# Optimization experiments

Measured on AMD Instinct MI355X. Metric: run time of the kernel, lower is better.

Reference implementation:

```python
import jax, jax.numpy as jnp
import numpy as np

B, T, D = 32, 4096, 512


def setup_inputs() -> dict:
    key = jax.random.key(0)
    k1, k2, k3 = jax.random.split(key, 3)
    inp = jax.random.normal(k1, (B, T, D), dtype=jnp.float32)
    # lengths in [1, T] so every row has at least one valid position
    lens = jax.random.randint(k2, (B,), 1, T + 1, dtype=jnp.int32)
    # matches nn.init.uniform_(slot_embedding, -1/d_hid, 1/d_hid)
    slot_embedding = jax.random.uniform(k3, (D,), dtype=jnp.float32,
                                        minval=-1.0 / D, maxval=1.0 / D)
    return {"inp": inp, "lens": lens, "slot_embedding": slot_embedding}


def reference(inp, lens, slot_embedding):
    # dropout p=0.0 -> identity (eval semantics)
    # scores[b, t] = <inp[b, t, :], slot_embedding>  -> [B, T]
    scores = jnp.einsum("btd,d->bt", inp, slot_embedding)
    # mask padded positions (t >= lens[b]) with -inf, as the per-sample loop does
    valid = jnp.arange(inp.shape[1], dtype=lens.dtype)[None, :] < lens[:, None]  # [B, T]
    scores = jnp.where(valid, scores, -jnp.inf)
    weights = jax.nn.softmax(scores, axis=1)  # [B, T]
    # context[b, d] = sum_t weights[b, t] * inp[b, t, d]
    context = jnp.einsum("bt,btd->bd", weights, inp)
    return context
```

## Files before the change

kernel.cpp:

```cpp
#include <hip/hip_runtime.h>
#include <math.h>


#define BB 32
#define TT 4096
#define DD 512

__global__ __launch_bounds__(256) void
slot_partial_kernel(const float* __restrict__ inp,
                    const int* __restrict__ lens,
                    const float* __restrict__ slot,
                    float* __restrict__ m_arr,
                    float* __restrict__ l_arr,
                    float* __restrict__ c_arr,
                    int CH, int R) {
    const int chunk = blockIdx.x;
    const int b     = blockIdx.y;
    const int tid   = threadIdx.x;
    const int wave  = tid >> 6;
    const int lane  = tid & 63;
    const int p     = b * CH + chunk;

    const int len = lens[b];
    const int cs  = chunk * R;
    const int ce  = min(cs + R, len);

    const float4 s0 = *reinterpret_cast<const float4*>(slot + lane * 4);
    const float4 s1 = *reinterpret_cast<const float4*>(slot + 256 + lane * 4);

    float  m = -INFINITY;
    float  l = 0.0f;
    float4 c0 = make_float4(0.f, 0.f, 0.f, 0.f);
    float4 c1 = make_float4(0.f, 0.f, 0.f, 0.f);

    const size_t baseB = (size_t)b * TT * DD;

    int t = cs + wave;
    if (t < ce) {
        const float* rp = inp + baseB + (size_t)t * DD;
        float4 a0 = *reinterpret_cast<const float4*>(rp + lane * 4);
        float4 a1 = *reinterpret_cast<const float4*>(rp + 256 + lane * 4);
        while (t < ce) {
            const int tn = t + 4;
            float4 n0, n1;
            if (tn < ce) {
                const float* rn = inp + baseB + (size_t)tn * DD;
                n0 = *reinterpret_cast<const float4*>(rn + lane * 4);
                n1 = *reinterpret_cast<const float4*>(rn + 256 + lane * 4);
            }
            float part = a0.x * s0.x + a0.y * s0.y + a0.z * s0.z + a0.w * s0.w
                       + a1.x * s1.x + a1.y * s1.y + a1.z * s1.z + a1.w * s1.w;
            #pragma unroll
            for (int off = 32; off >= 1; off >>= 1)
                part += __shfl_xor(part, off, 64);
            const float s = part;

            if (s > m) {
                const float alpha = __expf(m - s);
                l *= alpha;
                c0.x *= alpha; c0.y *= alpha; c0.z *= alpha; c0.w *= alpha;
                c1.x *= alpha; c1.y *= alpha; c1.z *= alpha; c1.w *= alpha;
                m = s;
            }
            const float w = __expf(s - m);
            l += w;
            c0.x += w * a0.x; c0.y += w * a0.y; c0.z += w * a0.z; c0.w += w * a0.w;
            c1.x += w * a1.x; c1.y += w * a1.y; c1.z += w * a1.z; c1.w += w * a1.w;

            a0 = n0; a1 = n1;
            t = tn;
        }
    }

    __shared__ float sm[4];
    __shared__ float sl[4];
    __shared__ float sc[4][DD];

    if (lane == 0) { sm[wave] = m; sl[wave] = l; }
    *reinterpret_cast<float4*>(&sc[wave][lane * 4])       = c0;
    *reinterpret_cast<float4*>(&sc[wave][256 + lane * 4]) = c1;
    __syncthreads();

    const float M = fmaxf(fmaxf(sm[0], sm[1]), fmaxf(sm[2], sm[3]));
    float aw[4];
    float L = 0.0f;
    #pragma unroll
    for (int w = 0; w < 4; ++w) {
        aw[w] = (sm[w] == -INFINITY) ? 0.0f : __expf(sm[w] - M);
        L += sl[w] * aw[w];
    }

    for (int d = tid; d < DD; d += 256) {
        const float acc = sc[0][d] * aw[0] + sc[1][d] * aw[1]
                        + sc[2][d] * aw[2] + sc[3][d] * aw[3];
        c_arr[(size_t)p * DD + d] = acc;
    }
    if (tid == 0) { m_arr[p] = M; l_arr[p] = L; }
}

__global__ __launch_bounds__(256) void
slot_combine_kernel(const float* __restrict__ m_arr,
                    const float* __restrict__ l_arr,
                    const float* __restrict__ c_arr,
                    float* __restrict__ out,
                    int CH) {
    const int b   = blockIdx.x;
    const int tid = threadIdx.x;

    __shared__ float sAlpha[64];

    float M = -INFINITY;
    for (int j = 0; j < CH; ++j) M = fmaxf(M, m_arr[b * CH + j]);

    if (tid < CH) {
        const float mj = m_arr[b * CH + tid];
        sAlpha[tid] = (mj == -INFINITY) ? 0.0f : __expf(mj - M);
    }
    __syncthreads();

    float L = 0.0f;
    for (int j = 0; j < CH; ++j) L += l_arr[b * CH + j] * sAlpha[j];
    const float invL = 1.0f / L;

    for (int d = tid; d < DD; d += 256) {
        float acc = 0.0f;
        for (int j = 0; j < CH; ++j)
            acc += c_arr[((size_t)b * CH + j) * DD + d] * sAlpha[j];
        out[b * DD + d] = acc * invL;
    }
}

extern "C" void kernel_launch(void* const* d_in, const int* in_sizes, int n_in,
                              void* d_out, int out_size, void* d_ws, size_t ws_size,
                              hipStream_t stream) {
    const float* inp  = (const float*)d_in[0];
    const int*   lens = (const int*)d_in[1];
    const float* slot = (const float*)d_in[2];
    float* out = (float*)d_out;

    int CH = 32;
    while (CH > 1 && (size_t)BB * CH * (2 + DD) * sizeof(float) > ws_size)
        CH >>= 1;
    const int R = TT / CH;
    const int P = BB * CH;

    float* m_arr = (float*)d_ws;
    float* l_arr = m_arr + P;
    float* c_arr = l_arr + P;

    dim3 grid1(CH, BB, 1);
    slot_partial_kernel<<<grid1, 256, 0, stream>>>(inp, lens, slot,
                                                   m_arr, l_arr, c_arr, CH, R);
    slot_combine_kernel<<<BB, 256, 0, stream>>>(m_arr, l_arr, c_arr, out, CH);
}
```

Before: 335.4 us.

## Give each wave a contiguous row range and process four rows per iteration

Each wave now takes a contiguous sub-range of the chunk instead of interleaved rows. It loads four rows at a time with a one-group-ahead prefetch and batches their four shuffle reductions together, applying the online-softmax rescale once per group. The chunk count rises to 64 to give more blocks, and the combine kernel switches to float2 loads. The goal is more memory-level parallelism and fewer serial shuffle and exp dependency chains, at the cost of higher register pressure. Combine work also grows with the larger chunk count.

Measured after the change: 334.7 us. No clear change (-0.2%).

```diff
diff --git a/kernel.cpp b/kernel.cpp
--- a/kernel.cpp
+++ b/kernel.cpp
@@ -13,7 +13,7 @@
                     float* __restrict__ m_arr,
                     float* __restrict__ l_arr,
                     float* __restrict__ c_arr,
-                    int CH, int R) {
+                    int CH, int R, int RW) {
     const int chunk = blockIdx.x;
     const int b     = blockIdx.y;
     const int tid   = threadIdx.x;
@@ -23,7 +23,8 @@
 
     const int len = lens[b];
     const int cs  = chunk * R;
-    const int ce  = min(cs + R, len);
+    const int ws_start = cs + wave * RW;
+    const int ws_end   = min(ws_start + RW, len);
 
     const float4 s0 = *reinterpret_cast<const float4*>(slot + lane * 4);
     const float4 s1 = *reinterpret_cast<const float4*>(slot + 256 + lane * 4);
@@ -33,42 +34,66 @@
     float4 c0 = make_float4(0.f, 0.f, 0.f, 0.f);
     float4 c1 = make_float4(0.f, 0.f, 0.f, 0.f);
 
-    const size_t baseB = (size_t)b * TT * DD;
+    const float* bp = inp + (size_t)b * TT * DD;
 
-    int t = cs + wave;
-    if (t < ce) {
-        const float* rp = inp + baseB + (size_t)t * DD;
-        float4 a0 = *reinterpret_cast<const float4*>(rp + lane * 4);
-        float4 a1 = *reinterpret_cast<const float4*>(rp + 256 + lane * 4);
-        while (t < ce) {
-            const int tn = t + 4;
-            float4 n0, n1;
-            if (tn < ce) {
-                const float* rn = inp + baseB + (size_t)tn * DD;
-                n0 = *reinterpret_cast<const float4*>(rn + lane * 4);
-                n1 = *reinterpret_cast<const float4*>(rn + 256 + lane * 4);
+    if (ws_start < ws_end) {
+        float4 a[4][2];
+        #pragma unroll
+        for (int r = 0; r < 4; ++r) {
+            const int t = min(ws_start + r, ws_end - 1);
+            const float* rp = bp + (size_t)t * DD + lane * 4;
+            a[r][0] = *reinterpret_cast<const float4*>(rp);
+            a[r][1] = *reinterpret_cast<const float4*>(rp + 256);
+        }
+        for (int g = ws_start; g < ws_end; g += 4) {
+            const int gn = g + 4;
+            float4 n[4][2];
+            if (gn < ws_end) {
+                #pragma unroll
+                for (int r = 0; r < 4; ++r) {
+                    const int t = min(gn + r, ws_end - 1);
+                    const float* rp = bp + (size_t)t * DD + lane * 4;
+                    n[r][0] = *reinterpret_cast<const float4*>(rp);
+                    n[r][1] = *reinterpret_cast<const float4*>(rp + 256);
+                }
             }
-            float part = a0.x * s0.x + a0.y * s0.y + a0.z * s0.z + a0.w * s0.w
-                       + a1.x * s1.x + a1.y * s1.y + a1.z * s1.z + a1.w * s1.w;
+            float sd[4];
             #pragma unroll
-            for (int off = 32; off >= 1; off >>= 1)
-                part += __shfl_xor(part, off, 64);
-            const float s = part;
+            for (int r = 0; r < 4; ++r) {
+                sd[r] = a[r][0].x * s0.x + a[r][0].y * s0.y
+                      + a[r][0].z * s0.z + a[r][0].w * s0.w
+                      + a[r][1].x * s1.x + a[r][1].y * s1.y
+                      + a[r][1].z * s1.z + a[r][1].w * s1.w;
+            }
+            #pragma unroll
+            for (int off = 32; off >= 1; off >>= 1) {
+                #pragma unroll
+                for (int r = 0; r < 4; ++r)
+                    sd[r] += __shfl_xor(sd[r], off, 64);
+            }
+            #pragma unroll
+            for (int r = 0; r < 4; ++r)
+                if (g + r >= ws_end) sd[r] = -INFINITY;
 
-            if (s > m) {
-                const float alpha = __expf(m - s);
+            const float gmax = fmaxf(fmaxf(sd[0], sd[1]), fmaxf(sd[2], sd[3]));
+            if (gmax > m) {
+                const float alpha = __expf(m - gmax);
                 l *= alpha;
                 c0.x *= alpha; c0.y *= alpha; c0.z *= alpha; c0.w *= alpha;
                 c1.x *= alpha; c1.y *= alpha; c1.z *= alpha; c1.w *= alpha;
-                m = s;
+                m = gmax;
             }
-            const float w = __expf(s - m);
-            l += w;
-            c0.x += w * a0.x; c0.y += w * a0.y; c0.z += w * a0.z; c0.w += w * a0.w;
-            c1.x += w * a1.x; c1.y += w * a1.y; c1.z += w * a1.z; c1.w += w * a1.w;
-
-            a0 = n0; a1 = n1;
-            t = tn;
+            #pragma unroll
+            for (int r = 0; r < 4; ++r) {
+                const float w = __expf(sd[r] - m);
+                l += w;
+                c0.x += w * a[r][0].x; c0.y += w * a[r][0].y;
+                c0.z += w * a[r][0].z; c0.w += w * a[r][0].w;
+                c1.x += w * a[r][1].x; c1.y += w * a[r][1].y;
+                c1.z += w * a[r][1].z; c1.w += w * a[r][1].w;
+            }
+            #pragma unroll
+            for (int r = 0; r < 4; ++r) { a[r][0] = n[r][0]; a[r][1] = n[r][1]; }
         }
     }
 
@@ -107,7 +132,7 @@
     const int b   = blockIdx.x;
     const int tid = threadIdx.x;
 
-    __shared__ float sAlpha[64];
+    __shared__ float sAlpha[256];
 
     float M = -INFINITY;
     for (int j = 0; j < CH; ++j) M = fmaxf(M, m_arr[b * CH + j]);
@@ -122,12 +147,16 @@
     for (int j = 0; j < CH; ++j) L += l_arr[b * CH + j] * sAlpha[j];
     const float invL = 1.0f / L;
 
-    for (int d = tid; d < DD; d += 256) {
-        float acc = 0.0f;
-        for (int j = 0; j < CH; ++j)
-            acc += c_arr[((size_t)b * CH + j) * DD + d] * sAlpha[j];
-        out[b * DD + d] = acc * invL;
+    const int d = tid * 2;
+    float2 acc = make_float2(0.f, 0.f);
+    for (int j = 0; j < CH; ++j) {
+        const float2 v = *reinterpret_cast<const float2*>(
+            c_arr + ((size_t)b * CH + j) * DD + d);
+        acc.x += v.x * sAlpha[j];
+        acc.y += v.y * sAlpha[j];
     }
+    out[b * DD + d]     = acc.x * invL;
+    out[b * DD + d + 1] = acc.y * invL;
 }
 
 extern "C" void kernel_launch(void* const* d_in, const int* in_sizes, int n_in,
@@ -138,11 +167,12 @@
     const float* slot = (const float*)d_in[2];
     float* out = (float*)d_out;
 
-    int CH = 32;
+    int CH = 64;
     while (CH > 1 && (size_t)BB * CH * (2 + DD) * sizeof(float) > ws_size)
         CH >>= 1;
-    const int R = TT / CH;
-    const int P = BB * CH;
+    const int R  = TT / CH;
+    const int RW = R / 4;
+    const int P  = BB * CH;
 
     float* m_arr = (float*)d_ws;
     float* l_arr = m_arr + P;
@@ -150,6 +180,7 @@
 
     dim3 grid1(CH, BB, 1);
     slot_partial_kernel<<<grid1, 256, 0, stream>>>(inp, lens, slot,
-                                                   m_arr, l_arr, c_arr, CH, R);
+                                                   m_arr, l_arr, c_arr,
+                                                   CH, R, RW);
     slot_combine_kernel<<<BB, 256, 0, stream>>>(m_arr, l_arr, c_arr, out, CH);
 }
```
